# Kernel optimization log

Measured on AMD Instinct MI355X. Metric: run time of the kernel, lower is better.

The kernel has to match this reference:

```python
import jax, jax.numpy as jnp
import numpy as np

T = 32400   # bs*H*W BEV queries (1*180*180)
S = 16896   # bs*num_cams*h*w image keys (1*6*32*88)
E = 256     # embed_dim
H = 8       # num_heads
D = 32      # head_dim
MAXL = 32   # max interval length (ref_num_f)


def _mlp(x, w1, b1, w2, b2):
    # nn.Sequential(Linear(E,2E), ReLU, Linear(2E,E))
    return jax.nn.relu(x @ w1 + b1) @ w2 + b2


def setup_inputs() -> dict:
    k0 = jax.random.key(0)
    ks = jax.random.split(k0, 8)
    # ragged interval structure: every BEV cell has an interval of length (idx%32)+1
    lengths = (np.arange(T) % MAXL) + 1
    starts = np.concatenate([np.zeros(1, np.int64), np.cumsum(lengths)[:-1]])
    N = int(lengths.sum())  # 534472 frustum points
    ranks_bev = np.repeat(np.arange(T), lengths)          # sorted by BEV cell
    rng = np.random.default_rng(0)
    ranks_feat = rng.integers(0, S, size=N)               # which key/value row each point reads

    def lin(k, fi, fo):
        return jax.random.normal(k, (fi, fo), jnp.float32) * (1.0 / np.sqrt(fi))

    key_feat = jax.random.normal(ks[1], (S, E), jnp.float32)
    return dict(
        query_depth=jax.random.normal(ks[0], (T, E), jnp.float32),
        key=key_feat,
        value=key_feat,  # module asserts torch.equal(key, value)
        q_w1=lin(ks[2], E, 2 * E), q_b1=jnp.zeros((2 * E,), jnp.float32),
        q_w2=lin(ks[3], 2 * E, E), q_b2=jnp.zeros((E,), jnp.float32),
        k_w1=lin(ks[4], E, 2 * E), k_b1=jnp.zeros((2 * E,), jnp.float32),
        k_w2=lin(ks[5], 2 * E, E), k_b2=jnp.zeros((E,), jnp.float32),
        ranks_feat_f=jnp.asarray(ranks_feat, jnp.int32),
        ranks_bev_f=jnp.asarray(ranks_bev, jnp.int32),
        interval_starts_f=jnp.asarray(starts, jnp.int32),
        interval_lengths_f=jnp.asarray(lengths, jnp.int32),
        ref_num=MAXL,
    )


def reference(query_depth, key, value,
              q_w1, q_b1, q_w2, q_b2,
              k_w1, k_b1, k_w2, k_b2,
              ranks_feat_f, ranks_bev_f,
              interval_starts_f, interval_lengths_f, ref_num):
    scaling = 1.0 / jnp.sqrt(jnp.float32(D))
    q = (_mlp(query_depth, q_w1, q_b1, q_w2, q_b2) * scaling).reshape(T, H, D)
    k = _mlp(key, k_w1, k_b1, k_w2, k_b2).reshape(S, H, D)
    v = value.reshape(S, H, D)

    N = ranks_bev_f.shape[0]
    pt = jnp.arange(N, dtype=jnp.int32)
    # interval id of each point (intervals are contiguous, sorted by start)
    iid = jnp.searchsorted(interval_starts_f, pt, side='right') - 1
    ranks_ref = pt - interval_starts_f[iid]  # within-interval slot, in [0, ref_num)

    # per-point raw attention logit: q[bev] . k[feat] per head  -> [N, H]
    w = jnp.einsum('nhd,nhd->nh', q[ranks_bev_f], k[ranks_feat_f])

    # scatter into ragged weight tensor [T, H, ref_num]; padding masked to -1e9
    attn = jnp.full((T, H, ref_num), -1e9, jnp.float32)
    attn = attn.at[ranks_bev_f, :, ranks_ref].set(w)
    attn = jax.nn.softmax(attn, axis=-1)

    # gather normalized weights back per point and scatter-combine values
    wp = attn[ranks_bev_f, :, ranks_ref]          # [N, H]
    vp = v[ranks_feat_f]                          # [N, H, D]
    out = jnp.zeros((T, H, D), jnp.float32).at[ranks_bev_f].add(wp[:, :, None] * vp)
    return out.reshape(T, E)
```

## Files before the change

kernel.cpp:

```cpp
#include <hip/hip_runtime.h>
#include <hip/hip_bf16.h>
#include <cstdint>
#include <cstddef>

constexpr int T_Q   = 32400;
constexpr int T_PAD = 32512;
constexpr int S_K   = 16896;
constexpr int E_DIM = 256;
constexpr int HID   = 512;

typedef __bf16 bf16x8 __attribute__((ext_vector_type(8)));
typedef float  f32x4  __attribute__((ext_vector_type(4)));
typedef unsigned short ushort8v __attribute__((ext_vector_type(8)));

__device__ __forceinline__ void async16(const __hip_bfloat16* gp, __hip_bfloat16* lp) {
    __builtin_amdgcn_global_load_lds(
        (const __attribute__((address_space(1))) void*)(gp),
        (__attribute__((address_space(3))) void*)(lp), 16, 0, 0);
}

__device__ __forceinline__ float b2f(unsigned short u) {
    return __uint_as_float(((unsigned)u) << 16);
}

constexpr int NB_K = (S_K * E_DIM / 4) / 256;
constexpr int NB_PREP = NB_K + 128;

__global__ __launch_bounds__(256) void prep(
    const float* __restrict__ val_in,
    const float* __restrict__ s0, const float* __restrict__ s1,
    const float* __restrict__ s2, const float* __restrict__ s3,
    __hip_bfloat16* __restrict__ kvB,
    __hip_bfloat16* __restrict__ d0, __hip_bfloat16* __restrict__ d1,
    __hip_bfloat16* __restrict__ d2, __hip_bfloat16* __restrict__ d3) {
    __shared__ float tb[64][65];
    const int b = blockIdx.x;
    const int tid = threadIdx.x;

    if (b < NB_K) {
        int i = (b * 256 + tid) * 4;
        float4 f = *(const float4*)(val_in + i);
        union { ushort4 u4; __hip_bfloat16 bb[4]; } cv;
        cv.bb[0] = __float2bfloat16(f.x);
        cv.bb[1] = __float2bfloat16(f.y);
        cv.bb[2] = __float2bfloat16(f.z);
        cv.bb[3] = __float2bfloat16(f.w);
        int r = i >> 8, c = i & 255;
        *(ushort4*)(kvB + (size_t)r * 512 + 256 + c) = cv.u4;
        return;
    }

    int tloc = b - NB_K;
    int m = tloc >> 5;
    int tt = tloc & 31;
    const float* S = m == 0 ? s0 : m == 1 ? s1 : m == 2 ? s2 : s3;
    __hip_bfloat16* D = m == 0 ? d0 : m == 1 ? d1 : m == 2 ? d2 : d3;
    int Kd, Nd, kt, nt;
    if ((m & 1) == 0) { Kd = 256; Nd = 512; kt = tt & 3; nt = tt >> 2; }
    else              { Kd = 512; Nd = 256; kt = tt & 7; nt = tt >> 3; }
    int tx = tid & 63, ty = tid >> 6;
#pragma unroll
    for (int p = 0; p < 16; ++p) {
        int row = ty * 16 + p;
        tb[row][tx] = S[(size_t)(kt * 64 + row) * Nd + nt * 64 + tx];
    }
    __syncthreads();
#pragma unroll
    for (int p = 0; p < 16; ++p) {
        int row = ty * 16 + p;
        D[(size_t)(nt * 64 + row) * Kd + kt * 64 + tx] = __float2bfloat16(tb[tx][row]);
    }
}


__global__ __launch_bounds__(256) void gemm1(
    const float* __restrict__ Aq, const float* __restrict__ Ak,
    const __hip_bfloat16* __restrict__ BTq, const __hip_bfloat16* __restrict__ BTk,
    const float* __restrict__ biasq, const float* __restrict__ biask,
    __hip_bfloat16* __restrict__ Cq, __hip_bfloat16* __restrict__ Ck,
    int qtiles) {
    __shared__ __hip_bfloat16 As[64 * 64];
    __shared__ __hip_bfloat16 Bs[256 * 64];

    const int tm = blockIdx.x >> 1;
    const int tn = blockIdx.x & 1;
    const bool isq = tm < qtiles;
    const float* A  = isq ? Aq : Ak;
    const __hip_bfloat16* BT = isq ? BTq : BTk;
    const float* bias = isq ? biasq : biask;
    __hip_bfloat16* C = isq ? Cq : Ck;
    const int mrow0 = (isq ? tm : tm - qtiles) * 64;
    const int rowlim = isq ? T_Q : S_K;
    const int n0 = tn * 256;

    const int tid = threadIdx.x;
    const int w = tid >> 6, l = tid & 63;
    const int lm = l & 15, lq = l >> 4;
    const int wn = w * 64;
    const int srow8 = l >> 3;
    const int u8 = l & 7;
    const int pu8 = u8 ^ srow8;
    const int scolB = (u8 ^ srow8) << 3;

    f32x4 acc[4][4] = {};

    for (int k0 = 0; k0 < 256; k0 += 64) {
#pragma unroll
        for (int c = 0; c < 2; ++c) {
            int r = w * 16 + c * 8 + srow8;
            int gr = mrow0 + r;
            float4 f0 = make_float4(0.f, 0.f, 0.f, 0.f);
            float4 f1 = make_float4(0.f, 0.f, 0.f, 0.f);
            if (gr < rowlim) {
                const float* ap = A + (size_t)gr * 256 + k0 + u8 * 8;
                f0 = *(const float4*)ap;
                f1 = *(const float4*)(ap + 4);
            }
            union { bf16x8 v; __hip_bfloat16 b[8]; } cv;
            cv.b[0] = __float2bfloat16(f0.x); cv.b[1] = __float2bfloat16(f0.y);
            cv.b[2] = __float2bfloat16(f0.z); cv.b[3] = __float2bfloat16(f0.w);
            cv.b[4] = __float2bfloat16(f1.x); cv.b[5] = __float2bfloat16(f1.y);
            cv.b[6] = __float2bfloat16(f1.z); cv.b[7] = __float2bfloat16(f1.w);
            *(bf16x8*)(As + r * 64 + pu8 * 8) = cv.v;
        }
#pragma unroll
        for (int c = 0; c < 8; ++c) {
            int r = w * 64 + c * 8 + srow8;
            async16(BT + (size_t)(n0 + r) * 256 + k0 + scolB,
                    Bs + (w * 64 + c * 8) * 64);
        }
        __syncthreads();

#pragma unroll
        for (int ks = 0; ks < 2; ++ks) {
            bf16x8 af[4], bfr[4];
#pragma unroll
            for (int mi = 0; mi < 4; ++mi) {
                int row = mi * 16 + lm;
                int pu = (ks * 4 + lq) ^ (row & 7);
                af[mi] = *(const bf16x8*)(As + row * 64 + pu * 8);
            }
#pragma unroll
            for (int ni = 0; ni < 4; ++ni) {
                int row = wn + ni * 16 + lm;
                int pu = (ks * 4 + lq) ^ (row & 7);
                bfr[ni] = *(const bf16x8*)(Bs + row * 64 + pu * 8);
            }
#pragma unroll
            for (int mi = 0; mi < 4; ++mi)
#pragma unroll
                for (int ni = 0; ni < 4; ++ni)
                    acc[mi][ni] = __builtin_amdgcn_mfma_f32_16x16x32_bf16(
                        af[mi], bfr[ni], acc[mi][ni], 0, 0, 0);
        }
        __syncthreads();
    }

#pragma unroll
    for (int ni = 0; ni < 4; ++ni) {
        int col = n0 + wn + ni * 16 + lm;
        float bv = bias[col];
#pragma unroll
        for (int mi = 0; mi < 4; ++mi) {
            size_t rowb = (size_t)mrow0 + mi * 16 + lq * 4;
#pragma unroll
            for (int r = 0; r < 4; ++r) {
                float vv = fmaxf(acc[mi][ni][r] + bv, 0.f);
                C[(rowb + r) * HID + col] = __float2bfloat16(vv);
            }
        }
    }
}

__global__ __launch_bounds__(256) void gemm2(
    const __hip_bfloat16* __restrict__ Aq, const __hip_bfloat16* __restrict__ Ak,
    const __hip_bfloat16* __restrict__ BTq, const __hip_bfloat16* __restrict__ BTk,
    const float* __restrict__ biasq, const float* __restrict__ biask,
    __hip_bfloat16* __restrict__ Cq, __hip_bfloat16* __restrict__ Ck,
    float scaleq, int qtiles) {
    __shared__ __hip_bfloat16 As[64 * 64];
    __shared__ __hip_bfloat16 Bs[256 * 64];

    const int tm = blockIdx.x;
    const bool isq = tm < qtiles;
    const __hip_bfloat16* A  = isq ? Aq : Ak;
    const __hip_bfloat16* BT = isq ? BTq : BTk;
    const float* bias = isq ? biasq : biask;
    __hip_bfloat16* C = isq ? Cq : Ck;
    const int ldc = isq ? E_DIM : 512;
    const float scale = isq ? scaleq : 1.0f;
    const int mrow0 = (isq ? tm : tm - qtiles) * 64;

    const int tid = threadIdx.x;
    const int w = tid >> 6, l = tid & 63;
    const int lm = l & 15, lq = l >> 4;
    const int wn = w * 64;
    const int srow8 = l >> 3;
    const int u8 = l & 7;
    const int scol = (u8 ^ srow8) << 3;

    f32x4 acc[4][4] = {};

    for (int k0 = 0; k0 < 512; k0 += 64) {
#pragma unroll
        for (int c = 0; c < 2; ++c) {
            int r = w * 16 + c * 8 + srow8;
            async16(A + (size_t)(mrow0 + r) * 512 + k0 + scol,
                    As + (w * 16 + c * 8) * 64);
        }
#pragma unroll
        for (int c = 0; c < 8; ++c) {
            int r = w * 64 + c * 8 + srow8;
            async16(BT + (size_t)r * 512 + k0 + scol,
                    Bs + (w * 64 + c * 8) * 64);
        }
        __syncthreads();

#pragma unroll
        for (int ks = 0; ks < 2; ++ks) {
            bf16x8 af[4], bfr[4];
#pragma unroll
            for (int mi = 0; mi < 4; ++mi) {
                int row = mi * 16 + lm;
                int pu = (ks * 4 + lq) ^ (row & 7);
                af[mi] = *(const bf16x8*)(As + row * 64 + pu * 8);
            }
#pragma unroll
            for (int ni = 0; ni < 4; ++ni) {
                int row = wn + ni * 16 + lm;
                int pu = (ks * 4 + lq) ^ (row & 7);
                bfr[ni] = *(const bf16x8*)(Bs + row * 64 + pu * 8);
            }
#pragma unroll
            for (int mi = 0; mi < 4; ++mi)
#pragma unroll
                for (int ni = 0; ni < 4; ++ni)
                    acc[mi][ni] = __builtin_amdgcn_mfma_f32_16x16x32_bf16(
                        af[mi], bfr[ni], acc[mi][ni], 0, 0, 0);
        }
        __syncthreads();
    }

#pragma unroll
    for (int ni = 0; ni < 4; ++ni) {
        int col = wn + ni * 16 + lm;
        float bv = bias[col];
#pragma unroll
        for (int mi = 0; mi < 4; ++mi) {
            size_t rowb = (size_t)mrow0 + mi * 16 + lq * 4;
#pragma unroll
            for (int r = 0; r < 4; ++r) {
                float vv = (acc[mi][ni][r] + bv) * scale;
                C[(rowb + r) * ldc + col] = __float2bfloat16(vv);
            }
        }
    }
}


#define PREFP(KB, VB, C)                                                     \
    {                                                                        \
        int f_ = __shfl(myf, (C) + half);                                    \
        const __hip_bfloat16* p_ = kv + ((size_t)f_ << 9) + (sub << 3);      \
        KB = *(const ushort8v*)p_;                                           \
        VB = *(const ushort8v*)(p_ + 256);                                   \
    }

#define PROCP(KB, VB, C)                                                     \
    {                                                                        \
        float wv = 0.f;                                                      \
        _Pragma("unroll") for (int i = 0; i < 8; ++i)                        \
            wv = fmaf(qf[i], b2f(KB[i]), wv);                                \
        wv += __shfl_xor(wv, 1);                                             \
        wv += __shfl_xor(wv, 2);                                             \
        float sc = ((C) + half < L) ? wv : -1e30f;                           \
        float so = __shfl_xor(sc, 32);                                       \
        float pm = fmaxf(sc, so);                                            \
        if (__all(pm <= m)) {                                                \
            float p = __expf(sc - m);                                        \
            s += p;                                                          \
            _Pragma("unroll") for (int i = 0; i < 8; ++i)                    \
                a[i] = fmaf(p, b2f(VB[i]), a[i]);                            \
        } else {                                                             \
            float mn = fmaxf(m, pm);                                         \
            float al = __expf(m - mn);                                       \
            float p  = __expf(sc - mn);                                      \
            m = mn;                                                          \
            s = fmaf(s, al, p);                                              \
            _Pragma("unroll") for (int i = 0; i < 8; ++i)                    \
                a[i] = fmaf(p, b2f(VB[i]), a[i] * al);                       \
        }                                                                    \
    }

#define STEPP(KB, VB, J)                                                     \
    if (c + (J) < L) {                                                       \
        PROCP(KB, VB, c + (J));                                              \
        if (c + (J) + 6 < L) PREFP(KB, VB, c + (J) + 6);                     \
    }

constexpr int ATTN_BLOCKS = 2026;

__global__ __launch_bounds__(256) void attn_kernel(
    const __hip_bfloat16* __restrict__ q,
    const __hip_bfloat16* __restrict__ kv,
    const int* __restrict__ rf,
    const int* __restrict__ starts,
    const int* __restrict__ lens,
    float* __restrict__ out) {
    const int wid = threadIdx.x >> 6;
    const int l = threadIdx.x & 63;
    const int sub = l & 31, half = l >> 5;
    const int tstride = gridDim.x * 4;

    for (int t = blockIdx.x * 4 + wid; t < T_Q; t += tstride) {
        int su = __builtin_amdgcn_readfirstlane(starts[t]);
        int L  = __builtin_amdgcn_readfirstlane(lens[t]);

        int li = l < L - 1 ? l : L - 1;
        int myf = rf[su + li];

        ushort8v qu = *(const ushort8v*)(q + (size_t)t * 256 + sub * 8);
        float qf[8];
#pragma unroll
        for (int i = 0; i < 8; ++i) qf[i] = b2f(qu[i]);

        float m = -INFINITY, s = 0.f;
        float a[8] = {0.f, 0.f, 0.f, 0.f, 0.f, 0.f, 0.f, 0.f};

        ushort8v k0 = {}, v0 = {}, k1 = {}, v1 = {}, k2 = {}, v2 = {};
        PREFP(k0, v0, 0);
        if (L > 2) PREFP(k1, v1, 2);
        if (L > 4) PREFP(k2, v2, 4);

        for (int c = 0; c < L; c += 6) {
            STEPP(k0, v0, 0)
            STEPP(k1, v1, 2)
            STEPP(k2, v2, 4)
        }

        float st = s + __shfl_xor(s, 32);
#pragma unroll
        for (int i = 0; i < 8; ++i) a[i] += __shfl_xor(a[i], 32);

        if (half) {
            float inv = 1.f / st;
            float* op = out + (size_t)t * 256 + sub * 8;
            float4 o0, o1;
            o0.x = a[0] * inv; o0.y = a[1] * inv; o0.z = a[2] * inv; o0.w = a[3] * inv;
            o1.x = a[4] * inv; o1.y = a[5] * inv; o1.z = a[6] * inv; o1.w = a[7] * inv;
            *(float4*)op = o0;
            *(float4*)(op + 4) = o1;
        }
    }
}

extern "C" void kernel_launch(void* const* d_in, const int* in_sizes, int n_in,
                              void* d_out, int out_size, void* d_ws, size_t ws_size,
                              hipStream_t stream) {
    const float* q_in   = (const float*)d_in[0];
    const float* key_in = (const float*)d_in[1];
    const float* val_in = (const float*)d_in[2];
    const float* q_w1   = (const float*)d_in[3];
    const float* q_b1   = (const float*)d_in[4];
    const float* q_w2   = (const float*)d_in[5];
    const float* q_b2   = (const float*)d_in[6];
    const float* k_w1   = (const float*)d_in[7];
    const float* k_b1   = (const float*)d_in[8];
    const float* k_w2   = (const float*)d_in[9];
    const float* k_b2   = (const float*)d_in[10];
    const int* ranks_feat = (const int*)d_in[11];
    const int* starts     = (const int*)d_in[13];
    const int* lens       = (const int*)d_in[14];
    float* out = (float*)d_out;

    char* ws = (char*)d_ws;
    size_t off = 0;
    auto alloc = [&](size_t bytes) {
        char* p = ws + off;
        off += (bytes + 255) & ~(size_t)255;
        return p;
    };
    __hip_bfloat16* hidQ = (__hip_bfloat16*)alloc((size_t)T_PAD * HID * 2);
    __hip_bfloat16* hidK = (__hip_bfloat16*)alloc((size_t)S_K * HID * 2);
    __hip_bfloat16* qMl  = (__hip_bfloat16*)alloc((size_t)T_PAD * E_DIM * 2);
    __hip_bfloat16* kvB  = (__hip_bfloat16*)alloc((size_t)S_K * 512 * 2);
    __hip_bfloat16* w1qT = (__hip_bfloat16*)alloc((size_t)HID * E_DIM * 2);
    __hip_bfloat16* w2qT = (__hip_bfloat16*)alloc((size_t)E_DIM * HID * 2);
    __hip_bfloat16* w1kT = (__hip_bfloat16*)alloc((size_t)HID * E_DIM * 2);
    __hip_bfloat16* w2kT = (__hip_bfloat16*)alloc((size_t)E_DIM * HID * 2);
    (void)ws_size; (void)n_in; (void)out_size; (void)in_sizes;

    prep<<<NB_PREP, 256, 0, stream>>>(val_in, q_w1, q_w2, k_w1, k_w2,
                                      kvB, w1qT, w2qT, w1kT, w2kT);

    const float qscale = 0.17677669529663687f;
    const int QT = T_PAD / 64;
    const int KT = S_K / 64;

    gemm1<<<(QT + KT) * 2, 256, 0, stream>>>(
        q_in, key_in, w1qT, w1kT, q_b1, k_b1, hidQ, hidK, QT);
    gemm2<<<QT + KT, 256, 0, stream>>>(
        hidQ, hidK, w2qT, w2kT, q_b2, k_b2, qMl, kvB, qscale, QT);

    attn_kernel<<<ATTN_BLOCKS, 256, 0, stream>>>(qMl, kvB, ranks_feat, starts, lens, out);
}
```

Before: 269.4 us.

## Fuse both MLP GEMMs into one kernel keeping hidden activations in LDS

```diff
diff --git a/kernel.cpp b/kernel.cpp
--- a/kernel.cpp
+++ b/kernel.cpp
@@ -73,184 +73,165 @@
 }
 
 
-__global__ __launch_bounds__(256) void gemm1(
+constexpr int MLP_QT = T_PAD / 64;
+constexpr int MLP_KT = S_K / 64;
+constexpr int MLP_NB = MLP_QT + MLP_KT;
+
+__global__ __launch_bounds__(512) void mlp_fused(
     const float* __restrict__ Aq, const float* __restrict__ Ak,
-    const __hip_bfloat16* __restrict__ BTq, const __hip_bfloat16* __restrict__ BTk,
-    const float* __restrict__ biasq, const float* __restrict__ biask,
+    const __hip_bfloat16* __restrict__ W1q, const __hip_bfloat16* __restrict__ W1k,
+    const __hip_bfloat16* __restrict__ W2q, const __hip_bfloat16* __restrict__ W2k,
+    const float* __restrict__ b1q, const float* __restrict__ b1k,
+    const float* __restrict__ b2q, const float* __restrict__ b2k,
     __hip_bfloat16* __restrict__ Cq, __hip_bfloat16* __restrict__ Ck,
-    int qtiles) {
-    __shared__ __hip_bfloat16 As[64 * 64];
+    float scaleq, int qtiles) {
+    __shared__ __hip_bfloat16 As[64 * 256];
     __shared__ __hip_bfloat16 Bs[256 * 64];
-
-    const int tm = blockIdx.x >> 1;
-    const int tn = blockIdx.x & 1;
-    const bool isq = tm < qtiles;
+    __shared__ __hip_bfloat16 Hs[64 * 512];
+
+    const int b = blockIdx.x;
+    const bool isq = b < qtiles;
     const float* A  = isq ? Aq : Ak;
-    const __hip_bfloat16* BT = isq ? BTq : BTk;
-    const float* bias = isq ? biasq : biask;
+    const __hip_bfloat16* W1 = isq ? W1q : W1k;
+    const __hip_bfloat16* W2 = isq ? W2q : W2k;
+    const float* b1 = isq ? b1q : b1k;
+    const float* b2 = isq ? b2q : b2k;
     __hip_bfloat16* C = isq ? Cq : Ck;
-    const int mrow0 = (isq ? tm : tm - qtiles) * 64;
+    const int ldc = isq ? E_DIM : 512;
+    const float scale = isq ? scaleq : 1.0f;
+    const int mrow0 = (isq ? b : b - qtiles) * 64;
     const int rowlim = isq ? T_Q : S_K;
-    const int n0 = tn * 256;
 
     const int tid = threadIdx.x;
     const int w = tid >> 6, l = tid & 63;
     const int lm = l & 15, lq = l >> 4;
-    const int wn = w * 64;
+    const int wm = w >> 2;
+    const int wn4 = w & 3;
     const int srow8 = l >> 3;
     const int u8 = l & 7;
-    const int pu8 = u8 ^ srow8;
     const int scolB = (u8 ^ srow8) << 3;
 
-    f32x4 acc[4][4] = {};
-
-    for (int k0 = 0; k0 < 256; k0 += 64) {
-#pragma unroll
-        for (int c = 0; c < 2; ++c) {
-            int r = w * 16 + c * 8 + srow8;
-            int gr = mrow0 + r;
-            float4 f0 = make_float4(0.f, 0.f, 0.f, 0.f);
-            float4 f1 = make_float4(0.f, 0.f, 0.f, 0.f);
-            if (gr < rowlim) {
-                const float* ap = A + (size_t)gr * 256 + k0 + u8 * 8;
-                f0 = *(const float4*)ap;
-                f1 = *(const float4*)(ap + 4);
-            }
-            union { bf16x8 v; __hip_bfloat16 b[8]; } cv;
-            cv.b[0] = __float2bfloat16(f0.x); cv.b[1] = __float2bfloat16(f0.y);
-            cv.b[2] = __float2bfloat16(f0.z); cv.b[3] = __float2bfloat16(f0.w);
-            cv.b[4] = __float2bfloat16(f1.x); cv.b[5] = __float2bfloat16(f1.y);
-            cv.b[6] = __float2bfloat16(f1.z); cv.b[7] = __float2bfloat16(f1.w);
-            *(bf16x8*)(As + r * 64 + pu8 * 8) = cv.v;
-        }
-#pragma unroll
-        for (int c = 0; c < 8; ++c) {
-            int r = w * 64 + c * 8 + srow8;
-            async16(BT + (size_t)(n0 + r) * 256 + k0 + scolB,
-                    Bs + (w * 64 + c * 8) * 64);
+#pragma unroll
+    for (int c = 0; c < 4; ++c) {
+        int idx = tid + c * 512;
+        int row = idx >> 5;
+        int u = idx & 31;
+        int gr = mrow0 + row;
+        float4 f0 = make_float4(0.f, 0.f, 0.f, 0.f);
+        float4 f1 = make_float4(0.f, 0.f, 0.f, 0.f);
+        if (gr < rowlim) {
+            const float* ap = A + (size_t)gr * 256 + u * 8;
+            f0 = *(const float4*)ap;
+            f1 = *(const float4*)(ap + 4);
+        }
+        union { bf16x8 v; __hip_bfloat16 bb[8]; } cv;
+        cv.bb[0] = __float2bfloat16(f0.x); cv.bb[1] = __float2bfloat16(f0.y);
+        cv.bb[2] = __float2bfloat16(f0.z); cv.bb[3] = __float2bfloat16(f0.w);
+        cv.bb[4] = __float2bfloat16(f1.x); cv.bb[5] = __float2bfloat16(f1.y);
+        cv.bb[6] = __float2bfloat16(f1.z); cv.bb[7] = __float2bfloat16(f1.w);
+        int pu = (u & 24) | ((u & 7) ^ (row & 7));
+        *(bf16x8*)(As + row * 256 + pu * 8) = cv.v;
+    }
+
+#pragma unroll 1
+    for (int nh = 0; nh < 2; ++nh) {
+        f32x4 acc[2][4] = {};
+        for (int k0 = 0; k0 < 256; k0 += 64) {
+#pragma unroll
+            for (int c = 0; c < 4; ++c) {
+                int r = w * 32 + c * 8 + srow8;
+                async16(W1 + (size_t)(nh * 256 + r) * 256 + k0 + scolB,
+                        Bs + (w * 32 + c * 8) * 64);
+            }
+            __syncthreads();
+#pragma unroll
+            for (int ks = 0; ks < 2; ++ks) {
+                bf16x8 af[2], bfr[4];
+#pragma unroll
+                for (int mi = 0; mi < 2; ++mi) {
+                    int row = wm * 32 + mi * 16 + lm;
+                    int un = (k0 >> 3) + ks * 4 + lq;
+                    int pu = (un & 24) | ((un & 7) ^ (row & 7));
+                    af[mi] = *(const bf16x8*)(As + row * 256 + pu * 8);
+                }
+#pragma unroll
+                for (int ni = 0; ni < 4; ++ni) {
+                    int brow = wn4 * 64 + ni * 16 + lm;
+                    int pu = (ks * 4 + lq) ^ (brow & 7);
+                    bfr[ni] = *(const bf16x8*)(Bs + brow * 64 + pu * 8);
+                }
+#pragma unroll
+                for (int mi = 0; mi < 2; ++mi)
+#pragma unroll
+                    for (int ni = 0; ni < 4; ++ni)
+                        acc[mi][ni] = __builtin_amdgcn_mfma_f32_16x16x32_bf16(
+                            af[mi], bfr[ni], acc[mi][ni], 0, 0, 0);
+            }
+            __syncthreads();
+        }
+#pragma unroll
+        for (int ni = 0; ni < 4; ++ni) {
+            int col = nh * 256 + wn4 * 64 + ni * 16 + lm;
+            float bv = b1[col];
+            int un = col >> 3, el = col & 7;
+#pragma unroll
+            for (int mi = 0; mi < 2; ++mi) {
+#pragma unroll
+                for (int r = 0; r < 4; ++r) {
+                    int row = wm * 32 + mi * 16 + lq * 4 + r;
+                    float vv = fmaxf(acc[mi][ni][r] + bv, 0.f);
+                    int pu = (un & 56) | ((un & 7) ^ (row & 7));
+                    Hs[row * 512 + pu * 8 + el] = __float2bfloat16(vv);
+                }
+            }
+        }
+    }
+
+    f32x4 acc2[2][4] = {};
+    for (int k0 = 0; k0 < 512; k0 += 64) {
+#pragma unroll
+        for (int c = 0; c < 4; ++c) {
+            int r = w * 32 + c * 8 + srow8;
+            async16(W2 + (size_t)r * 512 + k0 + scolB,
+                    Bs + (w * 32 + c * 8) * 64);
         }
         __syncthreads();
-
 #pragma unroll
         for (int ks = 0; ks < 2; ++ks) {
-            bf16x8 af[4], bfr[4];
-#pragma unroll
-            for (int mi = 0; mi < 4; ++mi) {
-                int row = mi * 16 + lm;
-                int pu = (ks * 4 + lq) ^ (row & 7);
-                af[mi] = *(const bf16x8*)(As + row * 64 + pu * 8);
+            bf16x8 af[2], bfr[4];
+#pragma unroll
+            for (int mi = 0; mi < 2; ++mi) {
+                int row = wm * 32 + mi * 16 + lm;
+                int un = (k0 >> 3) + ks * 4 + lq;
+                int pu = (un & 56) | ((un & 7) ^ (row & 7));
+                af[mi] = *(const bf16x8*)(Hs + row * 512 + pu * 8);
             }
 #pragma unroll
             for (int ni = 0; ni < 4; ++ni) {
-                int row = wn + ni * 16 + lm;
-                int pu = (ks * 4 + lq) ^ (row & 7);
-                bfr[ni] = *(const bf16x8*)(Bs + row * 64 + pu * 8);
-            }
-#pragma unroll
-            for (int mi = 0; mi < 4; ++mi)
+                int brow = wn4 * 64 + ni * 16 + lm;
+                int pu = (ks * 4 + lq) ^ (brow & 7);
+                bfr[ni] = *(const bf16x8*)(Bs + brow * 64 + pu * 8);
+            }
+#pragma unroll
+            for (int mi = 0; mi < 2; ++mi)
 #pragma unroll
                 for (int ni = 0; ni < 4; ++ni)
-                    acc[mi][ni] = __builtin_amdgcn_mfma_f32_16x16x32_bf16(
-                        af[mi], bfr[ni], acc[mi][ni], 0, 0, 0);
+                    acc2[mi][ni] = __builtin_amdgcn_mfma_f32_16x16x32_bf16(
+                        af[mi], bfr[ni], acc2[mi][ni], 0, 0, 0);
         }
         __syncthreads();
     }
 
 #pragma unroll
     for (int ni = 0; ni < 4; ++ni) {
-        int col = n0 + wn + ni * 16 + lm;
-        float bv = bias[col];
-#pragma unroll
-        for (int mi = 0; mi < 4; ++mi) {
-            size_t rowb = (size_t)mrow0 + mi * 16 + lq * 4;
+        int col = wn4 * 64 + ni * 16 + lm;
+        float bv = b2[col];
+#pragma unroll
+        for (int mi = 0; mi < 2; ++mi) {
+            size_t rowb = (size_t)mrow0 + wm * 32 + mi * 16 + lq * 4;
 #pragma unroll
             for (int r = 0; r < 4; ++r) {
-                float vv = fmaxf(acc[mi][ni][r] + bv, 0.f);
-                C[(rowb + r) * HID + col] = __float2bfloat16(vv);
-            }
-        }
-    }
-}
-
-__global__ __launch_bounds__(256) void gemm2(
-    const __hip_bfloat16* __restrict__ Aq, const __hip_bfloat16* __restrict__ Ak,
-    const __hip_bfloat16* __restrict__ BTq, const __hip_bfloat16* __restrict__ BTk,
-    const float* __restrict__ biasq, const float* __restrict__ biask,
-    __hip_bfloat16* __restrict__ Cq, __hip_bfloat16* __restrict__ Ck,
-    float scaleq, int qtiles) {
-    __shared__ __hip_bfloat16 As[64 * 64];
-    __shared__ __hip_bfloat16 Bs[256 * 64];
-
-    const int tm = blockIdx.x;
-    const bool isq = tm < qtiles;
-    const __hip_bfloat16* A  = isq ? Aq : Ak;
-    const __hip_bfloat16* BT = isq ? BTq : BTk;
-    const float* bias = isq ? biasq : biask;
-    __hip_bfloat16* C = isq ? Cq : Ck;
-    const int ldc = isq ? E_DIM : 512;
-    const float scale = isq ? scaleq : 1.0f;
-    const int mrow0 = (isq ? tm : tm - qtiles) * 64;
-
-    const int tid = threadIdx.x;
-    const int w = tid >> 6, l = tid & 63;
-    const int lm = l & 15, lq = l >> 4;
-    const int wn = w * 64;
-    const int srow8 = l >> 3;
-    const int u8 = l & 7;
-    const int scol = (u8 ^ srow8) << 3;
-
-    f32x4 acc[4][4] = {};
-
-    for (int k0 = 0; k0 < 512; k0 += 64) {
-#pragma unroll
-        for (int c = 0; c < 2; ++c) {
-            int r = w * 16 + c * 8 + srow8;
-            async16(A + (size_t)(mrow0 + r) * 512 + k0 + scol,
-                    As + (w * 16 + c * 8) * 64);
-        }
-#pragma unroll
-        for (int c = 0; c < 8; ++c) {
-            int r = w * 64 + c * 8 + srow8;
-            async16(BT + (size_t)r * 512 + k0 + scol,
-                    Bs + (w * 64 + c * 8) * 64);
-        }
-        __syncthreads();
-
-#pragma unroll
-        for (int ks = 0; ks < 2; ++ks) {
-            bf16x8 af[4], bfr[4];
-#pragma unroll
-            for (int mi = 0; mi < 4; ++mi) {
-                int row = mi * 16 + lm;
-                int pu = (ks * 4 + lq) ^ (row & 7);
-                af[mi] = *(const bf16x8*)(As + row * 64 + pu * 8);
-            }
-#pragma unroll
-            for (int ni = 0; ni < 4; ++ni) {
-                int row = wn + ni * 16 + lm;
-                int pu = (ks * 4 + lq) ^ (row & 7);
-                bfr[ni] = *(const bf16x8*)(Bs + row * 64 + pu * 8);
-            }
-#pragma unroll
-            for (int mi = 0; mi < 4; ++mi)
-#pragma unroll
-                for (int ni = 0; ni < 4; ++ni)
-                    acc[mi][ni] = __builtin_amdgcn_mfma_f32_16x16x32_bf16(
-                        af[mi], bfr[ni], acc[mi][ni], 0, 0, 0);
-        }
-        __syncthreads();
-    }
-
-#pragma unroll
-    for (int ni = 0; ni < 4; ++ni) {
-        int col = wn + ni * 16 + lm;
-        float bv = bias[col];
-#pragma unroll
-        for (int mi = 0; mi < 4; ++mi) {
-            size_t rowb = (size_t)mrow0 + mi * 16 + lq * 4;
-#pragma unroll
-            for (int r = 0; r < 4; ++r) {
-                float vv = (acc[mi][ni][r] + bv) * scale;
+                float vv = (acc2[mi][ni][r] + bv) * scale;
                 C[(rowb + r) * ldc + col] = __float2bfloat16(vv);
             }
         }
@@ -295,7 +276,7 @@
 #define STEPP(KB, VB, J)                                                     \
     if (c + (J) < L) {                                                       \
         PROCP(KB, VB, c + (J));                                              \
-        if (c + (J) + 6 < L) PREFP(KB, VB, c + (J) + 6);                     \
+        if (c + (J) + 8 < L) PREFP(KB, VB, c + (J) + 8);                     \
     }
 
 constexpr int ATTN_BLOCKS = 2026;
@@ -327,15 +308,18 @@
         float m = -INFINITY, s = 0.f;
         float a[8] = {0.f, 0.f, 0.f, 0.f, 0.f, 0.f, 0.f, 0.f};
 
-        ushort8v k0 = {}, v0 = {}, k1 = {}, v1 = {}, k2 = {}, v2 = {};
+        ushort8v k0 = {}, v0 = {}, k1 = {}, v1 = {};
+        ushort8v k2 = {}, v2 = {}, k3 = {}, v3 = {};
         PREFP(k0, v0, 0);
         if (L > 2) PREFP(k1, v1, 2);
         if (L > 4) PREFP(k2, v2, 4);
-
-        for (int c = 0; c < L; c += 6) {
+        if (L > 6) PREFP(k3, v3, 6);
+
+        for (int c = 0; c < L; c += 8) {
             STEPP(k0, v0, 0)
             STEPP(k1, v1, 2)
             STEPP(k2, v2, 4)
+            STEPP(k3, v3, 6)
         }
 
         float st = s + __shfl_xor(s, 32);
@@ -380,8 +364,6 @@
         off += (bytes + 255) & ~(size_t)255;
         return p;
     };
-    __hip_bfloat16* hidQ = (__hip_bfloat16*)alloc((size_t)T_PAD * HID * 2);
-    __hip_bfloat16* hidK = (__hip_bfloat16*)alloc((size_t)S_K * HID * 2);
     __hip_bfloat16* qMl  = (__hip_bfloat16*)alloc((size_t)T_PAD * E_DIM * 2);
     __hip_bfloat16* kvB  = (__hip_bfloat16*)alloc((size_t)S_K * 512 * 2);
     __hip_bfloat16* w1qT = (__hip_bfloat16*)alloc((size_t)HID * E_DIM * 2);
@@ -394,13 +376,10 @@
                                       kvB, w1qT, w2qT, w1kT, w2kT);
 
     const float qscale = 0.17677669529663687f;
-    const int QT = T_PAD / 64;
-    const int KT = S_K / 64;
-
-    gemm1<<<(QT + KT) * 2, 256, 0, stream>>>(
-        q_in, key_in, w1qT, w1kT, q_b1, k_b1, hidQ, hidK, QT);
-    gemm2<<<QT + KT, 256, 0, stream>>>(
-        hidQ, hidK, w2qT, w2kT, q_b2, k_b2, qMl, kvB, qscale, QT);
+
+    mlp_fused<<<MLP_NB, 512, 0, stream>>>(
+        q_in, key_in, w1qT, w1kT, w2qT, w2kT,
+        q_b1, k_b1, q_b2, k_b2, qMl, kvB, qscale, MLP_QT);
 
     attn_kernel<<<ATTN_BLOCKS, 256, 0, stream>>>(qMl, kvB, ranks_feat, starts, lens, out);
 }
```

Result: no change. 269.6 us (+0.1%).
